# Optimization experiments

Measured on AMD Instinct MI355X. Metric: run time of the kernel, lower is better.

Reference implementation:

```python
import jax, jax.numpy as jnp
import numpy as np

I, H, NH, A = 128, 2048, 2, 4   # input_size, hidden_size, n_hidden, alpha_dim
K = 2 * A * A                   # per-position theta entries
B = 8192


def make_masks():
    # MADE sequential-ordering masks, identical to DART.create_masks
    inp = np.arange(I)
    degrees = [inp] + [np.arange(H) % (I - 1) for _ in range(NH + 1)] + [np.arange(I) - 1]
    masks = [(d1[:, None] >= d0[None, :]).astype(np.float32)
             for d0, d1 in zip(degrees[:-1], degrees[1:])]
    # last mask repeated per theta entry: repeat(1, K).view(-1, H) == row-repeat
    masks[-1] = np.repeat(masks[-1], K, axis=0)
    return [jnp.asarray(m) for m in masks]


def setup_inputs() -> dict:
    key = jax.random.key(0)
    ks = jax.random.split(key, 5)
    x = jax.random.normal(ks[0], (B, I), dtype=jnp.float32)

    def lin(k, out_dim, in_dim):
        kw, kb = jax.random.split(k)
        s = 1.0 / np.sqrt(in_dim)
        W = jax.random.uniform(kw, (out_dim, in_dim), minval=-s, maxval=s, dtype=jnp.float32)
        b = jax.random.uniform(kb, (out_dim,), minval=-s, maxval=s, dtype=jnp.float32)
        return W, b

    W0, b0 = lin(ks[1], H, I)
    W1, b1 = lin(ks[2], H, H)
    W2, b2 = lin(ks[3], H, H)
    W3, b3 = lin(ks[4], I * K, H)
    return dict(x=x, W0=W0, b0=b0, W1=W1, b1=b1, W2=W2, b2=b2, W3=W3, b3=b3)


def logexpmm(a, b):
    # log-domain matmul: out[..., i, j] = logsumexp_k(a[..., i, k] + b[..., k, j])
    return jax.nn.logsumexp(a[..., :, :, None] + b[..., None, :, :], axis=-2)


def reference(x, W0, b0, W1, b1, W2, b2, W3, b3):
    m = make_masks()
    h = jax.nn.relu(x @ (m[0] * W0).T + b0)
    h = jax.nn.relu(h @ (m[1] * W1).T + b1)
    h = jax.nn.relu(h @ (m[2] * W2).T + b2)
    theta = (h @ (m[3] * W3).T + b3).reshape(-1, I, 2, A, A)
    mu, alpha = theta[:, :, 0], theta[:, :, 1]  # (B, I, A, A)

    LOG2PI = float(np.log(2.0 * np.pi))
    xe = x[:, :, None, None]
    # Normal(mu, exp(alpha)).log_prob(x) - log(alpha_dim)
    logp = (-0.5 * ((xe - mu) * jnp.exp(-alpha)) ** 2
            - alpha - 0.5 * LOG2PI - jnp.log(jnp.float32(A)))

    first = logp[:, 0, 0:1]        # (B, 1, A)
    last = logp[:, -1, :, 0:1]     # (B, A, 1)
    inner = jnp.swapaxes(logp[:, 1:-1], 0, 1)  # (I-2, B, A, A)

    def step(carry, mtx):
        return logexpmm(carry, mtx), None

    prod, _ = jax.lax.scan(step, inner[0], inner[1:])
    return logexpmm(first, logexpmm(prod, last))  # (B, 1, 1)
```

## Files before the change

### kernel.cpp

```cpp
#include <hip/hip_runtime.h>
#include <hip/hip_bf16.h>
#include <cstdint>
#include <cstddef>

#define AS1 __attribute__((address_space(1)))
#define AS3 __attribute__((address_space(3)))

typedef __bf16 bf16x8 __attribute__((ext_vector_type(8)));
typedef float  floatx4 __attribute__((ext_vector_type(4)));

__device__ __forceinline__ void load_lds16(const void* g, void* l) {
    __builtin_amdgcn_global_load_lds((AS1 void*)g, (AS3 void*)l, 16, 0, 0);
}

__device__ __forceinline__ float fexp2(float x) { return __builtin_amdgcn_exp2f(x); }
__device__ __forceinline__ float flog2(float x) { return __builtin_amdgcn_logf(x); }

__device__ __forceinline__ int resp_s(int p) {
    return p < 272 ? p / 17 : 16 + ((p - 272) >> 4);
}
__device__ __forceinline__ int invp_s(int p) {
    if (p < 272) { int d = p / 17; int r = p - d * 17;
                   return r < 16 ? d + r * 127 : 2032 + d; }
    int d = 16 + ((p - 272) >> 4); int j = (p - 272) & 15;
    return d + j * 127;
}
__device__ __forceinline__ int cnt_le(int D) {
    return D < 16 ? (D + 1) * 17 : 272 + ((D - 15) << 4);
}

__global__ __launch_bounds__(256)
void prep_all(const float* __restrict__ x,  const float* __restrict__ W0,
              const float* __restrict__ W1, const float* __restrict__ W2,
              const float* __restrict__ W3,
              __bf16* __restrict__ xb,  __bf16* __restrict__ w0m,
              __bf16* __restrict__ w1m, __bf16* __restrict__ w2m,
              __bf16* __restrict__ w3m)
{
    __shared__ float lds[2048];
    const int blk = blockIdx.x;
    const int tid = threadIdx.x;
    const int t8  = tid * 8;

    if (blk < 640) {
        bf16x8 o;
        if (blk < 512) {
            size_t base = (size_t)blk * 2048 + t8;
            floatx4 a = *(const floatx4*)(x + base);
            floatx4 b = *(const floatx4*)(x + base + 4);
#pragma unroll
            for (int j = 0; j < 4; ++j) { o[j] = (__bf16)a[j]; o[4 + j] = (__bf16)b[j]; }
            *(bf16x8*)(xb + base) = o;
        } else {
            long idx = (long)(blk - 512) * 2048 + t8;
            int p_n = (int)(idx >> 7);
            int c   = (int)(idx & 127);
            int dg  = resp_s(p_n);
            const float* s = W0 + (long)invp_s(p_n) * 128 + c;
            floatx4 a = *(const floatx4*)s;
            floatx4 b = *(const floatx4*)(s + 4);
#pragma unroll
            for (int j = 0; j < 8; ++j) {
                float v = j < 4 ? a[j] : b[j - 4];
                o[j] = (__bf16)((dg >= c + j) ? v : 0.0f);
            }
            *(bf16x8*)(w0m + idx) = o;
        }
        return;
    }

    const float* srow; __bf16* drow; int deg_n; bool strict;
    if (blk < 2688) {
        int p_n = blk - 640;
        srow = W1 + (size_t)invp_s(p_n) * 2048; drow = w1m + (size_t)p_n * 2048;
        deg_n = resp_s(p_n); strict = false;
    } else if (blk < 4736) {
        int p_n = blk - 2688;
        srow = W2 + (size_t)invp_s(p_n) * 2048; drow = w2m + (size_t)p_n * 2048;
        deg_n = resp_s(p_n); strict = false;
    } else {
        int n = blk - 4736;
        srow = W3 + (size_t)n * 2048; drow = w3m + (size_t)n * 2048;
        deg_n = n >> 5; strict = true;
    }
    floatx4 a = *(const floatx4*)(srow + t8);
    floatx4 b = *(const floatx4*)(srow + t8 + 4);
    *(floatx4*)&lds[t8]     = a;
    *(floatx4*)&lds[t8 + 4] = b;
    __syncthreads();
    bf16x8 o;
#pragma unroll
    for (int j = 0; j < 8; ++j) {
        int p = t8 + j;
        float v = lds[invp_s(p)];
        int dg = resp_s(p);
        bool keep = strict ? (deg_n > dg) : (deg_n >= dg);
        o[j] = (__bf16)(keep ? v : 0.0f);
    }
    *(bf16x8*)(drow + t8) = o;
}

template <bool RELU, bool OBF16, bool TLAYOUT, bool PERMBIAS, int LMODE>
__global__ __launch_bounds__(256, 4)
void gemm_bt(const __bf16* __restrict__ A, const __bf16* __restrict__ Bw,
             const float* __restrict__ bias, void* __restrict__ Cout,
             int N, int K)
{
    __shared__ __align__(16) __bf16 lsA[128 * 64];
    __shared__ __align__(16) __bf16 lsB[128 * 64];
    const int tid  = threadIdx.x;
    const int wave = tid >> 6;
    const int lane = tid & 63;
    const int bm = blockIdx.x;
    const int bn = (gridDim.y - 1) - blockIdx.y;
    const int wm = wave >> 1, wn = wave & 1;

    const int r8 = lane >> 3;
    const int cb = (lane & 7) ^ r8;
    const __bf16* gsrc[8];
    __bf16* ldst[8];
#pragma unroll
    for (int t = 0; t < 8; ++t) {
        int j = wave * 8 + t;
        if (j < 16) {
            int row = bm * 128 + j * 8 + r8;
            gsrc[t] = A + (size_t)row * K + cb * 8;
            ldst[t] = lsA + j * 512;
        } else {
            int jj = j - 16;
            int row = bn * 128 + jj * 8 + r8;
            gsrc[t] = Bw + (size_t)row * K + cb * 8;
            ldst[t] = lsB + jj * 512;
        }
    }

    const int fr  = lane & 15;
    const int ks  = lane >> 4;
    const int sx  = fr & 7;
    const int sl0 = ((ks)     ^ sx) * 8;
    const int sl1 = ((4 + ks) ^ sx) * 8;
    const __bf16* arow[4];
    const __bf16* brow[4];
#pragma unroll
    for (int i = 0; i < 4; ++i) {
        arow[i] = lsA + (wm * 64 + i * 16 + fr) * 64;
        brow[i] = lsB + (wn * 64 + i * 16 + fr) * 64;
    }

    floatx4 acc[4][4];
    const floatx4 vzero = {0.f, 0.f, 0.f, 0.f};
#pragma unroll
    for (int mi = 0; mi < 4; ++mi)
#pragma unroll
        for (int ni = 0; ni < 4; ++ni) acc[mi][ni] = vzero;

    const int nk = K >> 6;
    int limit;
    if (LMODE == 0)      limit = (cnt_le(resp_s(bn * 128 + 127)) + 63) >> 6;
    else if (LMODE == 1) { int D = 4 * bn + 2; if (D > 126) D = 126;
                           limit = (cnt_le(D) + 63) >> 6; }
    else                 limit = (resp_s(bn * 128 + 127) + 64) >> 6;
    if (limit > nk) limit = nk;

    for (int it = 0; it < limit; ++it) {
        const int kt = it << 6;
        __syncthreads();
#pragma unroll
        for (int t = 0; t < 8; ++t)
            load_lds16((const void*)(gsrc[t] + kt), (void*)ldst[t]);
        __syncthreads();
        bf16x8 af[4], bf[4];
#pragma unroll
        for (int i = 0; i < 4; ++i) af[i] = *(const bf16x8*)(arow[i] + sl0);
#pragma unroll
        for (int i = 0; i < 4; ++i) bf[i] = *(const bf16x8*)(brow[i] + sl0);
#pragma unroll
        for (int mi = 0; mi < 4; ++mi)
#pragma unroll
            for (int ni = 0; ni < 4; ++ni)
                acc[mi][ni] = __builtin_amdgcn_mfma_f32_16x16x32_bf16(
                    af[mi], bf[ni], acc[mi][ni], 0, 0, 0);
#pragma unroll
        for (int i = 0; i < 4; ++i) af[i] = *(const bf16x8*)(arow[i] + sl1);
#pragma unroll
        for (int i = 0; i < 4; ++i) bf[i] = *(const bf16x8*)(brow[i] + sl1);
#pragma unroll
        for (int mi = 0; mi < 4; ++mi)
#pragma unroll
            for (int ni = 0; ni < 4; ++ni)
                acc[mi][ni] = __builtin_amdgcn_mfma_f32_16x16x32_bf16(
                    af[mi], bf[ni], acc[mi][ni], 0, 0, 0);
    }

    const int cn  = lane & 15;
    const int cr4 = (lane >> 4) * 4;
#pragma unroll
    for (int ni = 0; ni < 4; ++ni) {
        int col = bn * 128 + wn * 64 + ni * 16 + cn;
        float bv = bias[PERMBIAS ? invp_s(col) : col];
#pragma unroll
        for (int mi = 0; mi < 4; ++mi) {
            int row0 = bm * 128 + wm * 64 + mi * 16 + cr4;
#pragma unroll
            for (int q = 0; q < 4; ++q) {
                float v = acc[mi][ni][q] + bv;
                if (RELU) v = fmaxf(v, 0.f);
                if (TLAYOUT) {
                    size_t addr = (size_t)(bm * 2 + wm) * ((size_t)N * 64)
                                + (size_t)col * 64 + (mi * 16 + cr4 + q);
                    ((__bf16*)Cout)[addr] = (__bf16)v;
                } else if (OBF16) {
                    ((__bf16*)Cout)[(size_t)(row0 + q) * N + col] = (__bf16)v;
                } else {
                    ((float*)Cout)[(size_t)(row0 + q) * N + col] = v;
                }
            }
        }
    }
}

__global__ __launch_bounds__(256)
void chain_seg(const __bf16* __restrict__ th2,
               const float* __restrict__ x,
               float* __restrict__ P)
{
    const int b = blockIdx.x * 256 + threadIdx.x;
    const int s = blockIdx.y;
    const int i0 = 1 + s * 7;
    const __bf16* tp = th2 + (size_t)(b >> 6) * (4096 * 64) + (b & 63)
                           + (size_t)i0 * 32 * 64;
    const float* xp = x + (size_t)b * 128 + i0;

    const float LOG2E = 1.4426950408889634f;
    const float C0    = 2.3052328943245633f;

    float M[4][4];
#pragma unroll
    for (int r = 0; r < 4; ++r)
#pragma unroll
        for (int c = 0; c < 4; ++c) M[r][c] = (r == c) ? 0.f : -1e30f;

    for (int ii = 0; ii < 7; ++ii) {
        float mu[16], al[16];
#pragma unroll
        for (int j = 0; j < 16; ++j) mu[j] = (float)tp[(size_t)j * 64];
#pragma unroll
        for (int j = 0; j < 16; ++j) al[j] = (float)tp[(size_t)(16 + j) * 64];
        float xv = xp[ii];
        tp += 32 * 64;
        float lp[16];
#pragma unroll
        for (int j = 0; j < 16; ++j) {
            float a = al[j];
            float e = fexp2(-a * LOG2E);
            float z = (xv - mu[j]) * e;
            lp[j] = (-0.5f * z * z - a - C0) * LOG2E;
        }
        float Mn[4][4];
#pragma unroll
        for (int r = 0; r < 4; ++r)
#pragma unroll
            for (int c = 0; c < 4; ++c) {
                float a0 = M[r][0] + lp[0 * 4 + c];
                float a1 = M[r][1] + lp[1 * 4 + c];
                float a2 = M[r][2] + lp[2 * 4 + c];
                float a3 = M[r][3] + lp[3 * 4 + c];
                float mx = fmaxf(fmaxf(a0, a1), fmaxf(a2, a3));
                float sm = fexp2(a0 - mx) + fexp2(a1 - mx) +
                           fexp2(a2 - mx) + fexp2(a3 - mx);
                Mn[r][c] = mx + flog2(sm);
            }
#pragma unroll
        for (int r = 0; r < 4; ++r)
#pragma unroll
            for (int c = 0; c < 4; ++c) M[r][c] = Mn[r][c];
    }

    float* pb = P + ((size_t)b * 18 + s) * 16;
#pragma unroll
    for (int r = 0; r < 4; ++r) {
        floatx4 o = {M[r][0], M[r][1], M[r][2], M[r][3]};
        *(floatx4*)(pb + r * 4) = o;
    }
}

__global__ __launch_bounds__(256)
void chain_fin(const __bf16* __restrict__ th2,
               const float* __restrict__ x,
               const float* __restrict__ P,
               float* __restrict__ out)
{
    const int tid  = threadIdx.x;
    const int lane = tid & 63;
    const int r    = lane & 3;
    const int l0   = lane & 60;
    const int b    = blockIdx.x * 64 + (tid >> 2);
    const __bf16* tb = th2 + (size_t)(b >> 6) * (4096 * 64) + (b & 63);

    const float LOG2E = 1.4426950408889634f;
    const float LN2   = 0.6931471805599453f;
    const float C0    = 2.3052328943245633f;

    const float* Pb = P + (size_t)b * 288;
    floatx4 m0 = *(const floatx4*)(Pb + r * 4);
    float M[4] = {m0[0], m0[1], m0[2], m0[3]};

#pragma unroll
    for (int s = 1; s < 18; ++s) {
        floatx4 lr = *(const floatx4*)(Pb + s * 16 + r * 4);
        float Mn[4];
#pragma unroll
        for (int c = 0; c < 4; ++c) {
            float a0 = M[0] + __shfl(lr[c], l0 + 0);
            float a1 = M[1] + __shfl(lr[c], l0 + 1);
            float a2 = M[2] + __shfl(lr[c], l0 + 2);
            float a3 = M[3] + __shfl(lr[c], l0 + 3);
            float mx = fmaxf(fmaxf(a0, a1), fmaxf(a2, a3));
            float sm = fexp2(a0 - mx) + fexp2(a1 - mx) + fexp2(a2 - mx) + fexp2(a3 - mx);
            Mn[c] = mx + flog2(sm);
        }
#pragma unroll
        for (int k = 0; k < 4; ++k) M[k] = Mn[k];
    }

    float xl = x[(size_t)b * 128 + 127];
    float a[4];
#pragma unroll
    for (int c = 0; c < 4; ++c) {
        float mu_ = (float)tb[(size_t)(4064 + c * 4) * 64];
        float al_ = (float)tb[(size_t)(4064 + 16 + c * 4) * 64];
        float e = fexp2(-al_ * LOG2E);
        float z = (xl - mu_) * e;
        float lp2 = (-0.5f * z * z - al_ - C0) * LOG2E;
        a[c] = M[c] + lp2;
    }
    float mx = fmaxf(fmaxf(a[0], a[1]), fmaxf(a[2], a[3]));
    float tr = mx + flog2(fexp2(a[0] - mx) + fexp2(a[1] - mx) +
                          fexp2(a[2] - mx) + fexp2(a[3] - mx));

    float x0  = x[(size_t)b * 128];
    float muf = (float)tb[(size_t)r * 64];
    float alf = (float)tb[(size_t)(16 + r) * 64];
    float ef = fexp2(-alf * LOG2E);
    float zf = (x0 - muf) * ef;
    float f2 = (-0.5f * zf * zf - alf - C0) * LOG2E;
    float v = f2 + tr;
    float m1 = fmaxf(v, __shfl_xor(v, 1));
    float m2 = fmaxf(m1, __shfl_xor(m1, 2));
    float sum = fexp2(v - m2);
    sum += __shfl_xor(sum, 1);
    sum += __shfl_xor(sum, 2);
    if (r == 0) out[b] = (m2 + flog2(sum)) * LN2;
}

extern "C" void kernel_launch(void* const* d_in, const int* in_sizes, int n_in,
                              void* d_out, int out_size, void* d_ws, size_t ws_size,
                              hipStream_t stream)
{
    (void)in_sizes; (void)n_in; (void)out_size; (void)ws_size;
    const float* x  = (const float*)d_in[0];
    const float* W0 = (const float*)d_in[1];
    const float* b0 = (const float*)d_in[2];
    const float* W1 = (const float*)d_in[3];
    const float* b1 = (const float*)d_in[4];
    const float* W2 = (const float*)d_in[5];
    const float* b2 = (const float*)d_in[6];
    const float* W3 = (const float*)d_in[7];
    const float* b3 = (const float*)d_in[8];

    char* ws = (char*)d_ws;
    size_t off = 0;
    auto alloc = [&](size_t bytes) { char* p = ws + off; off += bytes; return p; };
    __bf16* xb  = (__bf16*)alloc((size_t)8192 * 128 * 2);
    __bf16* w0m = (__bf16*)alloc((size_t)2048 * 128 * 2);
    __bf16* w1m = (__bf16*)alloc((size_t)2048 * 2048 * 2);
    __bf16* w2m = (__bf16*)alloc((size_t)2048 * 2048 * 2);
    __bf16* w3m = (__bf16*)alloc((size_t)4096 * 2048 * 2);
    __bf16* h1  = (__bf16*)alloc((size_t)8192 * 2048 * 2);
    __bf16* h2  = (__bf16*)alloc((size_t)8192 * 2048 * 2);
    __bf16* th  = (__bf16*)alloc((size_t)8192 * 4096 * 2);
    __bf16* h3  = h1;
    float*  P   = (float*)h2;

    prep_all<<<8832, 256, 0, stream>>>(x, W0, W1, W2, W3, xb, w0m, w1m, w2m, w3m);

    gemm_bt<true, true, false, true, 2><<<dim3(64, 16), 256, 0, stream>>>(
        xb, w0m, b0, h1, 2048, 128);
    gemm_bt<true, true, false, true, 0><<<dim3(64, 16), 256, 0, stream>>>(
        h1, w1m, b1, h2, 2048, 2048);
    gemm_bt<true, true, false, true, 0><<<dim3(64, 16), 256, 0, stream>>>(
        h2, w2m, b2, h3, 2048, 2048);
    gemm_bt<false, false, true, false, 1><<<dim3(64, 32), 256, 0, stream>>>(
        h3, w3m, b3, th, 4096, 2048);

    chain_seg<<<dim3(32, 18), 256, 0, stream>>>(th, x, P);
    chain_fin<<<128, 256, 0, stream>>>(th, x, P, (float*)d_out);
}
```

Measured before the change: 326.5 us.

## Switch GEMM to 32x32x16 MFMA and fuse chain into one LDS kernel

The GEMM inner loop moves from 16x16x32 to 32x32x16 bf16 MFMA tiles. The LDS swizzle gains an extra row-group XOR term, and the transposed-layout epilogue writes vectorized 4-wide bf16 stores. The two chain kernels merge into a single kernel that stages x in LDS, computes 14 segment products per batch element, and reduces them in shared memory, removing the global partial buffer and one launch. The workspace layout is also repacked into fixed offsets. The aim is fewer LDS reads per MFMA and less launch and global round-trip overhead, at the cost of lower chain-kernel parallelism (256 blocks, serial tail on 32 threads).

New measurement: 334.3 us. +2.4%, slower.

```diff
diff --git a/kernel.cpp b/kernel.cpp
--- a/kernel.cpp
+++ b/kernel.cpp
@@ -6,8 +6,10 @@
 #define AS1 __attribute__((address_space(1)))
 #define AS3 __attribute__((address_space(3)))
 
-typedef __bf16 bf16x8 __attribute__((ext_vector_type(8)));
+typedef __bf16 bf16x8  __attribute__((ext_vector_type(8)));
+typedef __bf16 bf16x4  __attribute__((ext_vector_type(4)));
 typedef float  floatx4 __attribute__((ext_vector_type(4)));
+typedef float  floatx16 __attribute__((ext_vector_type(16)));
 
 __device__ __forceinline__ void load_lds16(const void* g, void* l) {
     __builtin_amdgcn_global_load_lds((AS1 void*)g, (AS3 void*)l, 16, 0, 0);
@@ -15,6 +17,31 @@
 
 __device__ __forceinline__ float fexp2(float x) { return __builtin_amdgcn_exp2f(x); }
 __device__ __forceinline__ float flog2(float x) { return __builtin_amdgcn_logf(x); }
+
+#define LOG2E 1.4426950408889634f
+#define LN2   0.6931471805599453f
+#define C0K   2.3052328943245633f
+
+__device__ __forceinline__ float logp2(float xv, float mu, float al) {
+    float e = fexp2(-al * LOG2E);
+    float z = (xv - mu) * e;
+    return (-0.5f * z * z - al - C0K) * LOG2E;
+}
+__device__ __forceinline__ float lse4(float a0, float a1, float a2, float a3) {
+    float mx = fmaxf(fmaxf(a0, a1), fmaxf(a2, a3));
+    return mx + flog2(fexp2(a0 - mx) + fexp2(a1 - mx) +
+                      fexp2(a2 - mx) + fexp2(a3 - mx));
+}
+__device__ __forceinline__ void lmm4(const float* Aa, const float* Bb, float* D) {
+#pragma unroll
+    for (int r = 0; r < 4; ++r)
+#pragma unroll
+        for (int c = 0; c < 4; ++c)
+            D[r * 4 + c] = lse4(Aa[r * 4 + 0] + Bb[0 * 4 + c],
+                                Aa[r * 4 + 1] + Bb[1 * 4 + c],
+                                Aa[r * 4 + 2] + Bb[2 * 4 + c],
+                                Aa[r * 4 + 3] + Bb[3 * 4 + c]);
+}
 
 __device__ __forceinline__ int resp_s(int p) {
     return p < 272 ? p / 17 : 16 + ((p - 272) >> 4);
@@ -116,7 +143,6 @@
     const int wm = wave >> 1, wn = wave & 1;
 
     const int r8 = lane >> 3;
-    const int cb = (lane & 7) ^ r8;
     const __bf16* gsrc[8];
     __bf16* ldst[8];
 #pragma unroll
@@ -124,35 +150,39 @@
         int j = wave * 8 + t;
         if (j < 16) {
             int row = bm * 128 + j * 8 + r8;
+            int cb = (lane & 7) ^ r8 ^ (j & 3);
             gsrc[t] = A + (size_t)row * K + cb * 8;
             ldst[t] = lsA + j * 512;
         } else {
             int jj = j - 16;
             int row = bn * 128 + jj * 8 + r8;
+            int cb = (lane & 7) ^ r8 ^ (jj & 3);
             gsrc[t] = Bw + (size_t)row * K + cb * 8;
             ldst[t] = lsB + jj * 512;
         }
     }
 
-    const int fr  = lane & 15;
-    const int ks  = lane >> 4;
-    const int sx  = fr & 7;
-    const int sl0 = ((ks)     ^ sx) * 8;
-    const int sl1 = ((4 + ks) ^ sx) * 8;
-    const __bf16* arow[4];
-    const __bf16* brow[4];
-#pragma unroll
-    for (int i = 0; i < 4; ++i) {
-        arow[i] = lsA + (wm * 64 + i * 16 + fr) * 64;
-        brow[i] = lsB + (wn * 64 + i * 16 + fr) * 64;
-    }
-
-    floatx4 acc[4][4];
-    const floatx4 vzero = {0.f, 0.f, 0.f, 0.f};
-#pragma unroll
-    for (int mi = 0; mi < 4; ++mi)
-#pragma unroll
-        for (int ni = 0; ni < 4; ++ni) acc[mi][ni] = vzero;
+    const int fr = lane & 31;
+    const int kg = lane >> 5;
+    const int sw = (fr & 7) ^ (fr >> 3);
+    int off[4];
+#pragma unroll
+    for (int t = 0; t < 4; ++t) off[t] = ((t * 2 + kg) ^ sw) * 8;
+    const __bf16* arow[2];
+    const __bf16* brow[2];
+#pragma unroll
+    for (int i = 0; i < 2; ++i) {
+        arow[i] = lsA + (wm * 64 + i * 32 + fr) * 64;
+        brow[i] = lsB + (wn * 64 + i * 32 + fr) * 64;
+    }
+
+    floatx16 acc[2][2];
+#pragma unroll
+    for (int mi = 0; mi < 2; ++mi)
+#pragma unroll
+        for (int ni = 0; ni < 2; ++ni)
+#pragma unroll
+            for (int q = 0; q < 16; ++q) acc[mi][ni][q] = 0.f;
 
     const int nk = K >> 6;
     int limit;
@@ -169,188 +199,157 @@
         for (int t = 0; t < 8; ++t)
             load_lds16((const void*)(gsrc[t] + kt), (void*)ldst[t]);
         __syncthreads();
-        bf16x8 af[4], bf[4];
-#pragma unroll
-        for (int i = 0; i < 4; ++i) af[i] = *(const bf16x8*)(arow[i] + sl0);
-#pragma unroll
-        for (int i = 0; i < 4; ++i) bf[i] = *(const bf16x8*)(brow[i] + sl0);
-#pragma unroll
-        for (int mi = 0; mi < 4; ++mi)
-#pragma unroll
-            for (int ni = 0; ni < 4; ++ni)
-                acc[mi][ni] = __builtin_amdgcn_mfma_f32_16x16x32_bf16(
-                    af[mi], bf[ni], acc[mi][ni], 0, 0, 0);
-#pragma unroll
-        for (int i = 0; i < 4; ++i) af[i] = *(const bf16x8*)(arow[i] + sl1);
-#pragma unroll
-        for (int i = 0; i < 4; ++i) bf[i] = *(const bf16x8*)(brow[i] + sl1);
-#pragma unroll
-        for (int mi = 0; mi < 4; ++mi)
-#pragma unroll
-            for (int ni = 0; ni < 4; ++ni)
-                acc[mi][ni] = __builtin_amdgcn_mfma_f32_16x16x32_bf16(
-                    af[mi], bf[ni], acc[mi][ni], 0, 0, 0);
-    }
-
-    const int cn  = lane & 15;
-    const int cr4 = (lane >> 4) * 4;
-#pragma unroll
-    for (int ni = 0; ni < 4; ++ni) {
-        int col = bn * 128 + wn * 64 + ni * 16 + cn;
+#pragma unroll
+        for (int t = 0; t < 4; ++t) {
+            bf16x8 a0 = *(const bf16x8*)(arow[0] + off[t]);
+            bf16x8 a1 = *(const bf16x8*)(arow[1] + off[t]);
+            bf16x8 b0 = *(const bf16x8*)(brow[0] + off[t]);
+            bf16x8 b1 = *(const bf16x8*)(brow[1] + off[t]);
+            acc[0][0] = __builtin_amdgcn_mfma_f32_32x32x16_bf16(a0, b0, acc[0][0], 0, 0, 0);
+            acc[0][1] = __builtin_amdgcn_mfma_f32_32x32x16_bf16(a0, b1, acc[0][1], 0, 0, 0);
+            acc[1][0] = __builtin_amdgcn_mfma_f32_32x32x16_bf16(a1, b0, acc[1][0], 0, 0, 0);
+            acc[1][1] = __builtin_amdgcn_mfma_f32_32x32x16_bf16(a1, b1, acc[1][1], 0, 0, 0);
+        }
+    }
+
+    const int cn  = lane & 31;
+    const int rhi = (lane >> 5) * 4;
+#pragma unroll
+    for (int ni = 0; ni < 2; ++ni) {
+        int col = bn * 128 + wn * 64 + ni * 32 + cn;
         float bv = bias[PERMBIAS ? invp_s(col) : col];
 #pragma unroll
-        for (int mi = 0; mi < 4; ++mi) {
-            int row0 = bm * 128 + wm * 64 + mi * 16 + cr4;
-#pragma unroll
-            for (int q = 0; q < 4; ++q) {
-                float v = acc[mi][ni][q] + bv;
-                if (RELU) v = fmaxf(v, 0.f);
+        for (int mi = 0; mi < 2; ++mi) {
+#pragma unroll
+            for (int qg = 0; qg < 4; ++qg) {
+                int rowf = qg * 8 + rhi;
                 if (TLAYOUT) {
                     size_t addr = (size_t)(bm * 2 + wm) * ((size_t)N * 64)
-                                + (size_t)col * 64 + (mi * 16 + cr4 + q);
-                    ((__bf16*)Cout)[addr] = (__bf16)v;
-                } else if (OBF16) {
-                    ((__bf16*)Cout)[(size_t)(row0 + q) * N + col] = (__bf16)v;
+                                + (size_t)col * 64 + (mi * 32 + rowf);
+                    bf16x4 o;
+#pragma unroll
+                    for (int k = 0; k < 4; ++k) o[k] = (__bf16)(acc[mi][ni][qg * 4 + k] + bv);
+                    *(bf16x4*)((__bf16*)Cout + addr) = o;
                 } else {
-                    ((float*)Cout)[(size_t)(row0 + q) * N + col] = v;
+                    int row0 = bm * 128 + wm * 64 + mi * 32 + rowf;
+#pragma unroll
+                    for (int k = 0; k < 4; ++k) {
+                        float v = acc[mi][ni][qg * 4 + k] + bv;
+                        if (RELU) v = fmaxf(v, 0.f);
+                        if (OBF16) ((__bf16*)Cout)[(size_t)(row0 + k) * N + col] = (__bf16)v;
+                        else       ((float*)Cout)[(size_t)(row0 + k) * N + col] = v;
+                    }
                 }
             }
         }
     }
 }
 
-__global__ __launch_bounds__(256)
-void chain_seg(const __bf16* __restrict__ th2,
+__global__ __launch_bounds__(448)
+void chain_all(const __bf16* __restrict__ th2,
                const float* __restrict__ x,
-               float* __restrict__ P)
-{
-    const int b = blockIdx.x * 256 + threadIdx.x;
-    const int s = blockIdx.y;
-    const int i0 = 1 + s * 7;
-    const __bf16* tp = th2 + (size_t)(b >> 6) * (4096 * 64) + (b & 63)
-                           + (size_t)i0 * 32 * 64;
-    const float* xp = x + (size_t)b * 128 + i0;
-
-    const float LOG2E = 1.4426950408889634f;
-    const float C0    = 2.3052328943245633f;
-
-    float M[4][4];
-#pragma unroll
-    for (int r = 0; r < 4; ++r)
-#pragma unroll
-        for (int c = 0; c < 4; ++c) M[r][c] = (r == c) ? 0.f : -1e30f;
-
-    for (int ii = 0; ii < 7; ++ii) {
-        float mu[16], al[16];
-#pragma unroll
-        for (int j = 0; j < 16; ++j) mu[j] = (float)tp[(size_t)j * 64];
-#pragma unroll
-        for (int j = 0; j < 16; ++j) al[j] = (float)tp[(size_t)(16 + j) * 64];
-        float xv = xp[ii];
-        tp += 32 * 64;
-        float lp[16];
-#pragma unroll
-        for (int j = 0; j < 16; ++j) {
-            float a = al[j];
-            float e = fexp2(-a * LOG2E);
-            float z = (xv - mu[j]) * e;
-            lp[j] = (-0.5f * z * z - a - C0) * LOG2E;
-        }
-        float Mn[4][4];
-#pragma unroll
-        for (int r = 0; r < 4; ++r)
-#pragma unroll
-            for (int c = 0; c < 4; ++c) {
-                float a0 = M[r][0] + lp[0 * 4 + c];
-                float a1 = M[r][1] + lp[1 * 4 + c];
-                float a2 = M[r][2] + lp[2 * 4 + c];
-                float a3 = M[r][3] + lp[3 * 4 + c];
-                float mx = fmaxf(fmaxf(a0, a1), fmaxf(a2, a3));
-                float sm = fexp2(a0 - mx) + fexp2(a1 - mx) +
-                           fexp2(a2 - mx) + fexp2(a3 - mx);
-                Mn[r][c] = mx + flog2(sm);
-            }
-#pragma unroll
-        for (int r = 0; r < 4; ++r)
-#pragma unroll
-            for (int c = 0; c < 4; ++c) M[r][c] = Mn[r][c];
-    }
-
-    float* pb = P + ((size_t)b * 18 + s) * 16;
-#pragma unroll
-    for (int r = 0; r < 4; ++r) {
-        floatx4 o = {M[r][0], M[r][1], M[r][2], M[r][3]};
-        *(floatx4*)(pb + r * 4) = o;
-    }
-}
-
-__global__ __launch_bounds__(256)
-void chain_fin(const __bf16* __restrict__ th2,
-               const float* __restrict__ x,
-               const float* __restrict__ P,
                float* __restrict__ out)
 {
-    const int tid  = threadIdx.x;
-    const int lane = tid & 63;
-    const int r    = lane & 3;
-    const int l0   = lane & 60;
-    const int b    = blockIdx.x * 64 + (tid >> 2);
-    const __bf16* tb = th2 + (size_t)(b >> 6) * (4096 * 64) + (b & 63);
-
-    const float LOG2E = 1.4426950408889634f;
-    const float LN2   = 0.6931471805599453f;
-    const float C0    = 2.3052328943245633f;
-
-    const float* Pb = P + (size_t)b * 288;
-    floatx4 m0 = *(const floatx4*)(Pb + r * 4);
-    float M[4] = {m0[0], m0[1], m0[2], m0[3]};
-
-#pragma unroll
-    for (int s = 1; s < 18; ++s) {
-        floatx4 lr = *(const floatx4*)(Pb + s * 16 + r * 4);
-        float Mn[4];
-#pragma unroll
-        for (int c = 0; c < 4; ++c) {
-            float a0 = M[0] + __shfl(lr[c], l0 + 0);
-            float a1 = M[1] + __shfl(lr[c], l0 + 1);
-            float a2 = M[2] + __shfl(lr[c], l0 + 2);
-            float a3 = M[3] + __shfl(lr[c], l0 + 3);
-            float mx = fmaxf(fmaxf(a0, a1), fmaxf(a2, a3));
-            float sm = fexp2(a0 - mx) + fexp2(a1 - mx) + fexp2(a2 - mx) + fexp2(a3 - mx);
-            Mn[c] = mx + flog2(sm);
-        }
-#pragma unroll
-        for (int k = 0; k < 4; ++k) M[k] = Mn[k];
-    }
-
-    float xl = x[(size_t)b * 128 + 127];
-    float a[4];
-#pragma unroll
-    for (int c = 0; c < 4; ++c) {
-        float mu_ = (float)tb[(size_t)(4064 + c * 4) * 64];
-        float al_ = (float)tb[(size_t)(4064 + 16 + c * 4) * 64];
-        float e = fexp2(-al_ * LOG2E);
-        float z = (xl - mu_) * e;
-        float lp2 = (-0.5f * z * z - al_ - C0) * LOG2E;
-        a[c] = M[c] + lp2;
-    }
-    float mx = fmaxf(fmaxf(a[0], a[1]), fmaxf(a[2], a[3]));
-    float tr = mx + flog2(fexp2(a[0] - mx) + fexp2(a[1] - mx) +
-                          fexp2(a[2] - mx) + fexp2(a[3] - mx));
-
-    float x0  = x[(size_t)b * 128];
-    float muf = (float)tb[(size_t)r * 64];
-    float alf = (float)tb[(size_t)(16 + r) * 64];
-    float ef = fexp2(-alf * LOG2E);
-    float zf = (x0 - muf) * ef;
-    float f2 = (-0.5f * zf * zf - alf - C0) * LOG2E;
-    float v = f2 + tr;
-    float m1 = fmaxf(v, __shfl_xor(v, 1));
-    float m2 = fmaxf(m1, __shfl_xor(m1, 2));
-    float sum = fexp2(v - m2);
-    sum += __shfl_xor(sum, 1);
-    sum += __shfl_xor(sum, 2);
-    if (r == 0) out[b] = (m2 + flog2(sum)) * LN2;
+    __shared__ float xs[32 * 129];
+    __shared__ float Pl[32 * 238];
+    const int tid = threadIdx.x;
+    const int blk = blockIdx.x;
+
+    for (int idx = tid; idx < 4096; idx += 448) {
+        int bl = idx >> 7, i = idx & 127;
+        xs[bl * 129 + i] = x[(size_t)blk * 4096 + idx];
+    }
+    __syncthreads();
+
+    const int s  = tid >> 5;
+    const int bl = tid & 31;
+    const int b64 = (blk & 1) * 32 + bl;
+    const __bf16* tb = th2 + (size_t)(blk >> 1) * (4096 * 64) + b64;
+
+    {
+        const int i0 = 1 + s * 9;
+        const __bf16* tp = tb + (size_t)i0 * 32 * 64;
+        float M[4][4];
+#pragma unroll
+        for (int r = 0; r < 4; ++r)
+#pragma unroll
+            for (int c = 0; c < 4; ++c) M[r][c] = (r == c) ? 0.f : -1e30f;
+
+        for (int ii = 0; ii < 9; ++ii) {
+            float mu[16], al[16];
+#pragma unroll
+            for (int j = 0; j < 16; ++j) mu[j] = (float)tp[(size_t)j * 64];
+#pragma unroll
+            for (int j = 0; j < 16; ++j) al[j] = (float)tp[(size_t)(16 + j) * 64];
+            float xv = xs[bl * 129 + i0 + ii];
+            tp += 2048;
+            float lp[16];
+#pragma unroll
+            for (int j = 0; j < 16; ++j) lp[j] = logp2(xv, mu[j], al[j]);
+            float Mn[4][4];
+#pragma unroll
+            for (int r = 0; r < 4; ++r)
+#pragma unroll
+                for (int c = 0; c < 4; ++c)
+                    Mn[r][c] = lse4(M[r][0] + lp[0 + c], M[r][1] + lp[4 + c],
+                                    M[r][2] + lp[8 + c], M[r][3] + lp[12 + c]);
+#pragma unroll
+            for (int r = 0; r < 4; ++r)
+#pragma unroll
+                for (int c = 0; c < 4; ++c) M[r][c] = Mn[r][c];
+        }
+        float* pb = Pl + bl * 238 + s * 17;
+#pragma unroll
+        for (int r = 0; r < 4; ++r)
+#pragma unroll
+            for (int c = 0; c < 4; ++c) pb[r * 4 + c] = M[r][c];
+    }
+    __syncthreads();
+
+    float Q[16];
+    if (tid < 224) {
+        const float* base = Pl + bl * 238;
+        lmm4(base + (2 * s) * 17, base + (2 * s + 1) * 17, Q);
+    }
+    __syncthreads();
+    if (tid < 224) {
+        float* dst = Pl + bl * 238 + s * 17;
+#pragma unroll
+        for (int e = 0; e < 16; ++e) dst[e] = Q[e];
+    }
+    __syncthreads();
+
+    if (tid < 32) {
+        const float* base = Pl + tid * 238;
+        float M[16], T[16];
+#pragma unroll
+        for (int e = 0; e < 16; ++e) M[e] = base[e];
+#pragma unroll
+        for (int j = 1; j < 7; ++j) {
+            lmm4(M, base + j * 17, T);
+#pragma unroll
+            for (int e = 0; e < 16; ++e) M[e] = T[e];
+        }
+        const int bb64 = (blk & 1) * 32 + tid;
+        const __bf16* tbb = th2 + (size_t)(blk >> 1) * (4096 * 64) + bb64;
+        float x0 = xs[tid * 129 + 0];
+        float xl = xs[tid * 129 + 127];
+        float last[4], t4[4], f4[4];
+#pragma unroll
+        for (int c = 0; c < 4; ++c)
+            last[c] = logp2(xl, (float)tbb[(size_t)(4064 + c * 4) * 64],
+                                (float)tbb[(size_t)(4064 + 16 + c * 4) * 64]);
+#pragma unroll
+        for (int r = 0; r < 4; ++r)
+            t4[r] = lse4(M[r * 4 + 0] + last[0], M[r * 4 + 1] + last[1],
+                         M[r * 4 + 2] + last[2], M[r * 4 + 3] + last[3]);
+#pragma unroll
+        for (int r = 0; r < 4; ++r)
+            f4[r] = logp2(x0, (float)tbb[(size_t)r * 64],
+                              (float)tbb[(size_t)(16 + r) * 64]);
+        out[blk * 32 + tid] = LN2 * lse4(f4[0] + t4[0], f4[1] + t4[1],
+                                         f4[2] + t4[2], f4[3] + t4[3]);
+    }
 }
 
 extern "C" void kernel_launch(void* const* d_in, const int* in_sizes, int n_in,
@@ -369,18 +368,16 @@
     const float* b3 = (const float*)d_in[8];
 
     char* ws = (char*)d_ws;
-    size_t off = 0;
-    auto alloc = [&](size_t bytes) { char* p = ws + off; off += bytes; return p; };
-    __bf16* xb  = (__bf16*)alloc((size_t)8192 * 128 * 2);
-    __bf16* w0m = (__bf16*)alloc((size_t)2048 * 128 * 2);
-    __bf16* w1m = (__bf16*)alloc((size_t)2048 * 2048 * 2);
-    __bf16* w2m = (__bf16*)alloc((size_t)2048 * 2048 * 2);
-    __bf16* w3m = (__bf16*)alloc((size_t)4096 * 2048 * 2);
-    __bf16* h1  = (__bf16*)alloc((size_t)8192 * 2048 * 2);
-    __bf16* h2  = (__bf16*)alloc((size_t)8192 * 2048 * 2);
-    __bf16* th  = (__bf16*)alloc((size_t)8192 * 4096 * 2);
+    const size_t MB = 1024 * 1024;
+    __bf16* h2  = (__bf16*)(ws + 0);
+    __bf16* xb  = (__bf16*)(ws + 32 * MB);
+    __bf16* w0m = (__bf16*)(ws + 34 * MB);
+    __bf16* w1m = (__bf16*)(ws + 35 * MB);
+    __bf16* w2m = (__bf16*)(ws + 43 * MB);
+    __bf16* th  = (__bf16*)(ws + 0);
+    __bf16* w3m = (__bf16*)(ws + 64 * MB);
+    __bf16* h1  = (__bf16*)(ws + 80 * MB);
     __bf16* h3  = h1;
-    float*  P   = (float*)h2;
 
     prep_all<<<8832, 256, 0, stream>>>(x, W0, W1, W2, W3, xb, w0m, w1m, w2m, w3m);
 
@@ -393,6 +390,5 @@
     gemm_bt<false, false, true, false, 1><<<dim3(64, 32), 256, 0, stream>>>(
         h3, w3m, b3, th, 4096, 2048);
 
-    chain_seg<<<dim3(32, 18), 256, 0, stream>>>(th, x, P);
-    chain_fin<<<128, 256, 0, stream>>>(th, x, P, (float*)d_out);
-}
+    chain_all<<<256, 448, 0, stream>>>(th, x, (float*)d_out);
+}
```
